# Optimization experiments

Hardware: AMD Instinct MI355X
Metric: run time of the kernel (lower is better)

The kernel has to match this reference:

```python
import jax, jax.numpy as jnp
import numpy as np

B, N, D = 16, 2048, 64

def setup_inputs() -> dict:
    key = jax.random.key(0)
    kq, kk, kv = jax.random.split(key, 3)
    q = jax.random.normal(kq, (B, N, D), dtype=jnp.float32)
    k = jax.random.normal(kk, (B, N, D), dtype=jnp.float32)
    v = jax.random.normal(kv, (B, N, D), dtype=jnp.float32)
    scale = jnp.float32(1.0 / np.sqrt(D))  # canonical 1/sqrt(d_head)
    return {"q": q, "k": k, "v": v, "scale": scale}

def reference(q, k, v, scale):
    # attention = softmax((q @ k^T) * scale) over key axis; dropout p=0.0 is identity
    scores = jnp.einsum('bqd,bkd->bqk', q, k) * scale  # [B,N,N]
    attention = jax.nn.softmax(scores, axis=2)
    context = jnp.einsum('bqk,bkd->bqd', attention, v)  # [B,N,D]
    return (context, attention)
```

## Files before the change

kernel.cpp:

```cpp
#include <hip/hip_runtime.h>

#define Bb 16
#define Nn 2048
#define Dd 64

typedef __attribute__((ext_vector_type(8))) short s16x8;
typedef __attribute__((ext_vector_type(4))) short s16x4;
typedef __attribute__((ext_vector_type(4))) float fx4;

__device__ __forceinline__ unsigned short f2bf(float f) {
  union { float f; unsigned u; } v; v.f = f;
  unsigned r = v.u + 0x7FFFu + ((v.u >> 16) & 1u);
  return (unsigned short)(r >> 16);
}

__global__ void k_cvtK(const float* __restrict__ K, unsigned short* __restrict__ Kb) {
  int i = blockIdx.x * 256 + threadIdx.x;
  float4 f = ((const float4*)K)[i];
  ushort4 o;
  o.x = f2bf(f.x); o.y = f2bf(f.y); o.z = f2bf(f.z); o.w = f2bf(f.w);
  ((ushort4*)Kb)[i] = o;
}

__global__ void k_transV(const float* __restrict__ V, unsigned short* __restrict__ VT) {
  __shared__ float tile[32][33];
  int b = blockIdx.z;
  int j0 = blockIdx.x * 32, d0 = blockIdx.y * 32;
  int tx = threadIdx.x, ty = threadIdx.y;
  const float* Vb = V + (size_t)b * Nn * Dd;
  unsigned short* Tb = VT + (size_t)b * Dd * Nn;
  for (int r = ty; r < 32; r += 8)
    tile[r][tx] = Vb[(size_t)(j0 + r) * Dd + d0 + tx];
  __syncthreads();
  for (int r = ty; r < 32; r += 8)
    Tb[(size_t)(d0 + r) * Nn + j0 + tx] = f2bf(tile[tx][r]);
}

__global__ __launch_bounds__(256) void k_attn(
    const float* __restrict__ Q, const unsigned short* __restrict__ Kbf,
    const unsigned short* __restrict__ VTbf, const float* __restrict__ scale_p,
    float* __restrict__ ctx, float* att) {
  const int id = blockIdx.x;
  const int swz = ((id & 7) << 8) | (id >> 3);
  const int b = swz >> 7;
  const int q0 = (swz & 127) << 4;

  const int tid = threadIdx.x;
  const int wave = tid >> 6, lane = tid & 63;
  const int nl = lane & 15, quad = lane >> 4;
  const int qrow = q0 + nl;
  const float c2 = scale_p[0] * 1.44269504088896341f;

  __shared__ float sm[4][16];
  __shared__ float sl[4][16];
  __shared__ float obf[4 * 1024];

  s16x8 qb[2];
  {
    const float* qp = Q + ((size_t)b * Nn + qrow) * Dd + quad * 8;
#pragma unroll
    for (int kt = 0; kt < 2; ++kt) {
      float4 f0 = *(const float4*)(qp + kt * 32);
      float4 f1 = *(const float4*)(qp + kt * 32 + 4);
      s16x8 t;
      t[0] = (short)f2bf(f0.x); t[1] = (short)f2bf(f0.y);
      t[2] = (short)f2bf(f0.z); t[3] = (short)f2bf(f0.w);
      t[4] = (short)f2bf(f1.x); t[5] = (short)f2bf(f1.y);
      t[6] = (short)f2bf(f1.z); t[7] = (short)f2bf(f1.w);
      qb[kt] = t;
    }
  }
  const unsigned short* Kb = Kbf + (size_t)b * Nn * Dd;
  const unsigned short* VTb = VTbf + (size_t)b * Dd * Nn;
  float* attb = att + (size_t)b * Nn * Nn;

  float m = -3.0e38f, l = 0.0f;

  for (int t = 0; t < 4; ++t) {
    const int k0 = (wave * 4 + t) * 128;
    fx4 s[8];
#pragma unroll
    for (int nt = 0; nt < 8; ++nt) s[nt] = (fx4){0.f, 0.f, 0.f, 0.f};
#pragma unroll
    for (int nt = 0; nt < 8; ++nt) {
      const s16x8* ka =
          (const s16x8*)(Kb + ((size_t)(k0 + nt * 16 + nl)) * Dd + quad * 8);
      s[nt] = __builtin_amdgcn_mfma_f32_16x16x32_bf16(ka[0], qb[0], s[nt], 0, 0, 0);
      s[nt] = __builtin_amdgcn_mfma_f32_16x16x32_bf16(ka[4], qb[1], s[nt], 0, 0, 0);
    }
    float x0 = s[0][0], x1 = s[0][1], x2 = s[0][2], x3 = s[0][3];
#pragma unroll
    for (int nt = 1; nt < 8; ++nt) {
      x0 = fmaxf(x0, s[nt][0]); x1 = fmaxf(x1, s[nt][1]);
      x2 = fmaxf(x2, s[nt][2]); x3 = fmaxf(x3, s[nt][3]);
    }
    float lm = fmaxf(fmaxf(x0, x1), fmaxf(x2, x3));
    float mn = fmaxf(m, lm * c2);
    float a0 = 0.f, a1 = 0.f, a2 = 0.f, a3 = 0.f;
#pragma unroll
    for (int nt = 0; nt < 8; ++nt) {
      a0 += exp2f(fmaf(s[nt][0], c2, -mn));
      a1 += exp2f(fmaf(s[nt][1], c2, -mn));
      a2 += exp2f(fmaf(s[nt][2], c2, -mn));
      a3 += exp2f(fmaf(s[nt][3], c2, -mn));
    }
    float ls = (a0 + a1) + (a2 + a3);
    l = l * exp2f(m - mn) + ls;
    m = mn;
  }
#pragma unroll
  for (int mask = 16; mask <= 32; mask <<= 1) {
    float om = __shfl_xor(m, mask, 64);
    float ol = __shfl_xor(l, mask, 64);
    float mn = fmaxf(m, om);
    l = l * exp2f(m - mn) + ol * exp2f(om - mn);
    m = mn;
  }
  if (lane < 16) { sm[wave][lane] = m; sl[wave][lane] = l; }
  __syncthreads();
  float rinv;
  {
    float M = sm[0][nl], L = sl[0][nl];
#pragma unroll
    for (int j = 1; j < 4; ++j) {
      float mj = sm[j][nl], lj = sl[j][nl];
      float mn = fmaxf(M, mj);
      L = L * exp2f(M - mn) + lj * exp2f(mj - mn);
      M = mn;
    }
    m = M;
    rinv = 1.0f / L;
  }

  fx4 o[4];
#pragma unroll
  for (int d = 0; d < 4; ++d) o[d] = (fx4){0.f, 0.f, 0.f, 0.f};

  float* myob = obf + wave * 1024;

  for (int t = 0; t < 4; ++t) {
    const int k0 = (wave * 4 + t) * 128;
    fx4 s[8];
#pragma unroll
    for (int nt = 0; nt < 8; ++nt) s[nt] = (fx4){0.f, 0.f, 0.f, 0.f};
#pragma unroll
    for (int nt = 0; nt < 8; ++nt) {
      const s16x8* ka =
          (const s16x8*)(Kb + ((size_t)(k0 + nt * 16 + nl)) * Dd + quad * 8);
      s[nt] = __builtin_amdgcn_mfma_f32_16x16x32_bf16(ka[0], qb[0], s[nt], 0, 0, 0);
      s[nt] = __builtin_amdgcn_mfma_f32_16x16x32_bf16(ka[4], qb[1], s[nt], 0, 0, 0);
    }
#pragma unroll
    for (int c = 0; c < 2; ++c) {
#pragma unroll
      for (int n4 = 0; n4 < 4; ++n4) {
        const int nt = c * 4 + n4;
        s16x4 vb[4];
#pragma unroll
        for (int ntd = 0; ntd < 4; ++ntd)
          vb[ntd] = *(const s16x4*)(VTb + ((size_t)(ntd * 16 + nl)) * Nn + k0 +
                                    nt * 16 + quad * 4);
        fx4 p;
#pragma unroll
        for (int r = 0; r < 4; ++r)
          p[r] = exp2f(fmaf(s[nt][r], c2, -m)) * rinv;
        {
          const int su = (n4 * 4 + quad) ^ (nl & 7);
          *(fx4*)&myob[nl * 64 + su * 4] = p;
        }
        s16x4 pa;
        pa[0] = (short)f2bf(p[0]); pa[1] = (short)f2bf(p[1]);
        pa[2] = (short)f2bf(p[2]); pa[3] = (short)f2bf(p[3]);
#pragma unroll
        for (int ntd = 0; ntd < 4; ++ntd)
          o[ntd] = __builtin_amdgcn_mfma_f32_16x16x16bf16_1k(pa, vb[ntd], o[ntd], 0, 0, 0);
      }
      asm volatile("s_waitcnt lgkmcnt(0)" ::: "memory");
      {
        const int rl = lane >> 4, un = lane & 15;
#pragma unroll
        for (int rb = 0; rb < 4; ++rb) {
          const int row = rb * 4 + rl;
          const int su = un ^ (row & 7);
          fx4 val = *(const fx4*)&myob[row * 64 + su * 4];
          __builtin_nontemporal_store(
              val, (fx4*)(attb + (size_t)(q0 + row) * Nn + k0 + c * 64 + un * 4));
        }
      }
    }
  }

#pragma unroll
  for (int ntd = 0; ntd < 4; ++ntd)
#pragma unroll
    for (int r = 0; r < 4; ++r) {
      const int row = quad * 4 + r;
      const int unit = ntd * 4 + (nl >> 2);
      const int su = unit ^ (row & 7);
      myob[row * 64 + su * 4 + (nl & 3)] = o[ntd][r];
    }
  __syncthreads();
  {
    const int row = tid >> 4;
    const int un = tid & 15;
    const int su = un ^ (row & 7);
    fx4 a = *(const fx4*)&obf[row * 64 + su * 4];
#pragma unroll
    for (int j = 1; j < 4; ++j) {
      fx4 tt = *(const fx4*)&obf[j * 1024 + row * 64 + su * 4];
      a[0] += tt[0]; a[1] += tt[1]; a[2] += tt[2]; a[3] += tt[3];
    }
    *(fx4*)(ctx + ((size_t)b * Nn + q0 + row) * Dd + un * 4) = a;
  }
}

extern "C" void kernel_launch(void* const* d_in, const int* in_sizes, int n_in,
                              void* d_out, int out_size, void* d_ws, size_t ws_size,
                              hipStream_t stream) {
  const float* q = (const float*)d_in[0];
  const float* k = (const float*)d_in[1];
  const float* v = (const float*)d_in[2];
  const float* scale = (const float*)d_in[3];

  float* ctx = (float*)d_out;
  float* att = ctx + (size_t)Bb * Nn * Dd;

  unsigned short* Kbf = (unsigned short*)d_ws;
  unsigned short* VTbf = Kbf + (size_t)Bb * Nn * Dd;

  hipLaunchKernelGGL(k_cvtK, dim3((Bb * Nn * Dd) / (256 * 4)), dim3(256), 0, stream,
                     k, Kbf);
  hipLaunchKernelGGL(k_transV, dim3(Nn / 32, Dd / 32, Bb), dim3(32, 8), 0, stream,
                     v, VTbf);
  hipLaunchKernelGGL(k_attn, dim3(Bb * Nn / 16), dim3(256), 0, stream,
                     q, Kbf, VTbf, scale, ctx, att);
}
```

Measured before the change: 491.2 us.

## Stage bf16 probabilities in LDS for wider PV MFMA and store attention directly

The P·V product now uses the 16x16x32 bf16 MFMA instead of the 16x16x16 one. Probabilities are packed to bf16 and written into a swizzled per-wave LDS buffer, then read back in the A-operand layout, with V loaded as 8-element vectors. Attention probabilities are stored straight from registers with nontemporal stores, replacing the fp32 LDS round-trip and its waitcnt. The aim is fewer MFMA issues and less LDS traffic. The cost is that each row's global stores are now 64-byte segments per quad rather than full contiguous rows, which may coalesce less well.

After: 444.1 us. 9.6% less time.

```diff
diff --git a/kernel.cpp b/kernel.cpp
--- a/kernel.cpp
+++ b/kernel.cpp
@@ -5,7 +5,6 @@
 #define Dd 64
 
 typedef __attribute__((ext_vector_type(8))) short s16x8;
-typedef __attribute__((ext_vector_type(4))) short s16x4;
 typedef __attribute__((ext_vector_type(4))) float fx4;
 
 __device__ __forceinline__ unsigned short f2bf(float f) {
@@ -39,7 +38,7 @@
 __global__ __launch_bounds__(256) void k_attn(
     const float* __restrict__ Q, const unsigned short* __restrict__ Kbf,
     const unsigned short* __restrict__ VTbf, const float* __restrict__ scale_p,
-    float* __restrict__ ctx, float* att) {
+    float* __restrict__ ctx, float* __restrict__ att) {
   const int id = blockIdx.x;
   const int swz = ((id & 7) << 8) | (id >> 3);
   const int b = swz >> 7;
@@ -53,7 +52,8 @@
 
   __shared__ float sm[4][16];
   __shared__ float sl[4][16];
-  __shared__ float obf[4 * 1024];
+  __shared__ __align__(16) float obf[4 * 1024];
+  char* pbw = (char*)obf + wave * 4096;
 
   s16x8 qb[2];
   {
@@ -136,8 +136,6 @@
 #pragma unroll
   for (int d = 0; d < 4; ++d) o[d] = (fx4){0.f, 0.f, 0.f, 0.f};
 
-  float* myob = obf + wave * 1024;
-
   for (int t = 0; t < 4; ++t) {
     const int k0 = (wave * 4 + t) * 128;
     fx4 s[8];
@@ -151,54 +149,48 @@
       s[nt] = __builtin_amdgcn_mfma_f32_16x16x32_bf16(ka[4], qb[1], s[nt], 0, 0, 0);
     }
 #pragma unroll
-    for (int c = 0; c < 2; ++c) {
-#pragma unroll
-      for (int n4 = 0; n4 < 4; ++n4) {
-        const int nt = c * 4 + n4;
-        s16x4 vb[4];
-#pragma unroll
-        for (int ntd = 0; ntd < 4; ++ntd)
-          vb[ntd] = *(const s16x4*)(VTb + ((size_t)(ntd * 16 + nl)) * Nn + k0 +
-                                    nt * 16 + quad * 4);
-        fx4 p;
-#pragma unroll
-        for (int r = 0; r < 4; ++r)
-          p[r] = exp2f(fmaf(s[nt][r], c2, -m)) * rinv;
-        {
-          const int su = (n4 * 4 + quad) ^ (nl & 7);
-          *(fx4*)&myob[nl * 64 + su * 4] = p;
-        }
-        s16x4 pa;
-        pa[0] = (short)f2bf(p[0]); pa[1] = (short)f2bf(p[1]);
-        pa[2] = (short)f2bf(p[2]); pa[3] = (short)f2bf(p[3]);
-#pragma unroll
-        for (int ntd = 0; ntd < 4; ++ntd)
-          o[ntd] = __builtin_amdgcn_mfma_f32_16x16x16bf16_1k(pa, vb[ntd], o[ntd], 0, 0, 0);
+    for (int nt = 0; nt < 8; ++nt) {
+#pragma unroll
+      for (int r = 0; r < 4; ++r)
+        s[nt][r] = exp2f(fmaf(s[nt][r], c2, -m)) * rinv;
+      unsigned long long pk =
+          (unsigned long long)f2bf(s[nt][0]) |
+          ((unsigned long long)f2bf(s[nt][1]) << 16) |
+          ((unsigned long long)f2bf(s[nt][2]) << 32) |
+          ((unsigned long long)f2bf(s[nt][3]) << 48);
+      *(unsigned long long*)(pbw + nl * 256 +
+                             ((nt * 32 + quad * 8) ^ ((nl & 7) << 4))) = pk;
+    }
+#pragma unroll
+    for (int kt = 0; kt < 4; ++kt) {
+      s16x8 pa = *(const s16x8*)(pbw + nl * 256 +
+                                 ((kt * 64 + quad * 16) ^ ((nl & 7) << 4)));
+#pragma unroll
+      for (int ntd = 0; ntd < 4; ++ntd) {
+        s16x8 vb = *(const s16x8*)(VTb + ((size_t)(ntd * 16 + nl)) * Nn + k0 +
+                                   kt * 32 + quad * 8);
+        o[ntd] = __builtin_amdgcn_mfma_f32_16x16x32_bf16(pa, vb, o[ntd], 0, 0, 0);
       }
-      asm volatile("s_waitcnt lgkmcnt(0)" ::: "memory");
-      {
-        const int rl = lane >> 4, un = lane & 15;
-#pragma unroll
-        for (int rb = 0; rb < 4; ++rb) {
-          const int row = rb * 4 + rl;
-          const int su = un ^ (row & 7);
-          fx4 val = *(const fx4*)&myob[row * 64 + su * 4];
-          __builtin_nontemporal_store(
-              val, (fx4*)(attb + (size_t)(q0 + row) * Nn + k0 + c * 64 + un * 4));
-        }
+    }
+    __builtin_amdgcn_sched_barrier(0);
+#pragma unroll
+    for (int nt = 0; nt < 8; ++nt)
+      __builtin_nontemporal_store(
+          s[nt], (fx4*)(attb + (size_t)qrow * Nn + k0 + nt * 16 + quad * 4));
+  }
+
+  {
+    float* myob = obf + wave * 1024;
+#pragma unroll
+    for (int ntd = 0; ntd < 4; ++ntd)
+#pragma unroll
+      for (int r = 0; r < 4; ++r) {
+        const int row = quad * 4 + r;
+        const int unit = ntd * 4 + (nl >> 2);
+        const int su = unit ^ (row & 7);
+        myob[row * 64 + su * 4 + (nl & 3)] = o[ntd][r];
       }
-    }
-  }
-
-#pragma unroll
-  for (int ntd = 0; ntd < 4; ++ntd)
-#pragma unroll
-    for (int r = 0; r < 4; ++r) {
-      const int row = quad * 4 + r;
-      const int unit = ntd * 4 + (nl >> 2);
-      const int su = unit ^ (row & 7);
-      myob[row * 64 + su * 4 + (nl & 3)] = o[ntd][r];
-    }
+  }
   __syncthreads();
   {
     const int row = tid >> 4;
```
